# Kernel optimization log

Measured on AMD Instinct MI355X. Metric: run time of the kernel, lower is better.

The kernel has to match this reference:

```python
import jax, jax.numpy as jnp
import numpy as np

IN_FEATURES = 4096
LOCAL_FEATURES = 128
KERNEL_SIZE = 64
STRIDE = 32
FOLD_NUM = (IN_FEATURES - KERNEL_SIZE) // STRIDE + 1  # 127
BATCH = 4096


def setup_inputs() -> dict:
    key = jax.random.key(0)
    kx, kw, kb = jax.random.split(key, 3)
    x = jax.random.normal(kx, (BATCH, IN_FEATURES), dtype=jnp.float32)
    # Per-window linear weights: torch Linear weight is [out, in] = [local_features, kernel_size]
    bound = 1.0 / np.sqrt(KERNEL_SIZE)
    W = jax.random.uniform(kw, (FOLD_NUM, LOCAL_FEATURES, KERNEL_SIZE),
                           dtype=jnp.float32, minval=-bound, maxval=bound)
    b = jax.random.uniform(kb, (FOLD_NUM, LOCAL_FEATURES),
                           dtype=jnp.float32, minval=-bound, maxval=bound)
    return {"x": x, "W": W, "b": b}


def reference(x, W, b) -> jnp.ndarray:
    # Unfold: windows[f, k] = x[:, f*stride + k] -> [B, FOLD_NUM, KERNEL_SIZE]
    idx = jnp.arange(FOLD_NUM)[:, None] * STRIDE + jnp.arange(KERNEL_SIZE)[None, :]
    windows = x[:, idx]  # [B, F, K]
    # Batched per-window linear: out[b, f, l] = sum_k windows[b,f,k] * W[f,l,k] + b[f,l]
    out = jnp.einsum('bfk,flk->bfl', windows, W) + b[None, :, :]
    # torch.cat along dim 1 over fold index == reshape [B, F*L]
    return out.reshape(x.shape[0], FOLD_NUM * LOCAL_FEATURES)
```

## Files before the change

kernel.cpp:

```cpp
#include <hip/hip_runtime.h>
#include <hip/hip_bf16.h>

#define IN_F 4096
#define LOCAL_F 128
#define KSZ 64
#define STRIDE_ 32
#define FOLDS 127
#define BATCH_ 4096
#define OUT_F (FOLDS * LOCAL_F)
#define WN (FOLDS * LOCAL_F * KSZ)

#define BM 64
#define NF 4
#define XCOLS (NF * STRIDE_ + (KSZ - STRIDE_))
#define LDSP 168

typedef __attribute__((ext_vector_type(8))) short bf16x8;
typedef __attribute__((ext_vector_type(8))) unsigned short u16x8;
typedef __attribute__((ext_vector_type(4))) float f32x4;

__device__ __forceinline__ unsigned short f2bf(float f) {
    unsigned u = __builtin_bit_cast(unsigned, f);
    u += 0x7fffu + ((u >> 16) & 1u);
    return (unsigned short)(u >> 16);
}

__global__ __launch_bounds__(256)
void wprep_kernel(const float* __restrict__ W, unsigned short* __restrict__ Wbf) {
    int i = (blockIdx.x * 256 + threadIdx.x) * 8;
    if (i >= WN) return;
    float4 a = *reinterpret_cast<const float4*>(W + i);
    float4 c = *reinterpret_cast<const float4*>(W + i + 4);
    u16x8 s;
    s[0] = f2bf(a.x); s[1] = f2bf(a.y); s[2] = f2bf(a.z); s[3] = f2bf(a.w);
    s[4] = f2bf(c.x); s[5] = f2bf(c.y); s[6] = f2bf(c.z); s[7] = f2bf(c.w);
    *reinterpret_cast<u16x8*>(Wbf + i) = s;
}

template<bool WB>
__global__ __launch_bounds__(256, 2)
void local_linear_kernel(const float* __restrict__ x,
                         const float* __restrict__ Wf32,
                         const unsigned short* __restrict__ Wbf,
                         const float* __restrict__ b,
                         float* __restrict__ out) {
    __shared__ unsigned short xs[BM][LDSP];

    const int bg = blockIdx.x;
    const int fg = blockIdx.y;
    const int row0 = bg * BM;
    const int col0 = fg * (NF * STRIDE_);

    const int t = threadIdx.x;

    #pragma unroll
    for (int it = 0; it < (BM * (XCOLS / 4)) / 256; ++it) {
        int i  = t + it * 256;
        int r  = i / (XCOLS / 4);
        int c4 = i - r * (XCOLS / 4);
        int gcol = col0 + c4 * 4;
        float4 v = make_float4(0.f, 0.f, 0.f, 0.f);
        if (gcol < IN_F) {
            v = *reinterpret_cast<const float4*>(x + (size_t)(row0 + r) * IN_F + gcol);
        }
        ushort4 s;
        s.x = f2bf(v.x); s.y = f2bf(v.y); s.z = f2bf(v.z); s.w = f2bf(v.w);
        *reinterpret_cast<ushort4*>(&xs[r][c4 * 4]) = s;
    }
    __syncthreads();

    const int wave = t >> 6;
    const int lane = t & 63;
    const int f = fg * NF + wave;
    if (f >= FOLDS) return;

    const int l16 = lane & 15;
    const int g   = lane >> 4;

    f32x4 acc[4][8];
    #pragma unroll
    for (int mt = 0; mt < 4; ++mt)
        #pragma unroll
        for (int nt = 0; nt < 8; ++nt)
            acc[mt][nt] = (f32x4){0.f, 0.f, 0.f, 0.f};

    const int fcol = wave * STRIDE_;

    #pragma unroll
    for (int ks = 0; ks < 2; ++ks) {
        bf16x8 wf[8];
        #pragma unroll
        for (int nt = 0; nt < 8; ++nt) {
            if (WB) {
                wf[nt] = *reinterpret_cast<const bf16x8*>(
                    Wbf + ((size_t)f * LOCAL_F + nt * 16 + l16) * KSZ + ks * 32 + g * 8);
            } else {
                const float* p = Wf32 + ((size_t)f * LOCAL_F + nt * 16 + l16) * KSZ + ks * 32 + g * 8;
                float4 va = *reinterpret_cast<const float4*>(p);
                float4 vb = *reinterpret_cast<const float4*>(p + 4);
                bf16x8 w8;
                w8[0] = (short)f2bf(va.x); w8[1] = (short)f2bf(va.y);
                w8[2] = (short)f2bf(va.z); w8[3] = (short)f2bf(va.w);
                w8[4] = (short)f2bf(vb.x); w8[5] = (short)f2bf(vb.y);
                w8[6] = (short)f2bf(vb.z); w8[7] = (short)f2bf(vb.w);
                wf[nt] = w8;
            }
        }
        bf16x8 af[4];
        #pragma unroll
        for (int mt = 0; mt < 4; ++mt) {
            af[mt] = *reinterpret_cast<const bf16x8*>(&xs[mt * 16 + l16][fcol + ks * 32 + g * 8]);
        }
        #pragma unroll
        for (int mt = 0; mt < 4; ++mt)
            #pragma unroll
            for (int nt = 0; nt < 8; ++nt)
                acc[mt][nt] = __builtin_amdgcn_mfma_f32_16x16x32_bf16(wf[nt], af[mt], acc[mt][nt], 0, 0, 0);
    }

    f32x4 bv[8];
    #pragma unroll
    for (int nt = 0; nt < 8; ++nt)
        bv[nt] = *reinterpret_cast<const f32x4*>(b + (size_t)f * LOCAL_F + nt * 16 + 4 * g);

    #pragma unroll
    for (int mt = 0; mt < 4; ++mt) {
        float* orow = out + (size_t)(row0 + mt * 16 + l16) * OUT_F + f * LOCAL_F + 4 * g;
        #pragma unroll
        for (int nt = 0; nt < 8; ++nt) {
            f32x4 v = acc[mt][nt] + bv[nt];
            *reinterpret_cast<f32x4*>(orow + nt * 16) = v;
        }
    }
}

extern "C" void kernel_launch(void* const* d_in, const int* in_sizes, int n_in,
                              void* d_out, int out_size, void* d_ws, size_t ws_size,
                              hipStream_t stream) {
    const float* x = (const float*)d_in[0];
    const float* W = (const float*)d_in[1];
    const float* b = (const float*)d_in[2];
    float* out = (float*)d_out;
    dim3 grid(BATCH_ / BM, (FOLDS + NF - 1) / NF);

    if (ws_size >= (size_t)WN * sizeof(unsigned short)) {
        unsigned short* Wbf = (unsigned short*)d_ws;
        wprep_kernel<<<(WN / 8 + 255) / 256, 256, 0, stream>>>(W, Wbf);
        local_linear_kernel<true><<<grid, 256, 0, stream>>>(x, W, Wbf, b, out);
    } else {
        local_linear_kernel<false><<<grid, 256, 0, stream>>>(x, W, nullptr, b, out);
    }
}
```

Baseline: 117.7 us.

## Split each fold across two waves, halve folds per block, use nontemporal stores

Each block now covers 2 folds instead of 4, and each fold's 128 output features are split across two waves of 64 features each. This halves the accumulator registers per wave, and the launch bound is raised to 4 blocks per CU to get more occupancy and latency hiding. Output stores become nontemporal to avoid polluting the cache with the large streamed output. The trade-off is more redundant x loading and bf16 conversion, since the x overlap between neighbouring folds is now shared by fewer folds per block. The fp32-weight fallback path is removed and the workspace is assumed to be large enough.

New measurement: 103.0 us. -12.5%, faster.

```diff
diff --git a/kernel.cpp b/kernel.cpp
--- a/kernel.cpp
+++ b/kernel.cpp
@@ -11,9 +11,9 @@
 #define WN (FOLDS * LOCAL_F * KSZ)
 
 #define BM 64
-#define NF 4
+#define NF 2
 #define XCOLS (NF * STRIDE_ + (KSZ - STRIDE_))
-#define LDSP 168
+#define LDSP 104
 
 typedef __attribute__((ext_vector_type(8))) short bf16x8;
 typedef __attribute__((ext_vector_type(8))) unsigned short u16x8;
@@ -37,10 +37,8 @@
     *reinterpret_cast<u16x8*>(Wbf + i) = s;
 }
 
-template<bool WB>
-__global__ __launch_bounds__(256, 2)
+__global__ __launch_bounds__(256, 4)
 void local_linear_kernel(const float* __restrict__ x,
-                         const float* __restrict__ Wf32,
                          const unsigned short* __restrict__ Wbf,
                          const float* __restrict__ b,
                          float* __restrict__ out) {
@@ -71,65 +69,53 @@
 
     const int wave = t >> 6;
     const int lane = t & 63;
-    const int f = fg * NF + wave;
+    const int fold = wave >> 1;
+    const int h    = wave & 1;
+    const int f = fg * NF + fold;
     if (f >= FOLDS) return;
 
     const int l16 = lane & 15;
     const int g   = lane >> 4;
 
-    f32x4 acc[4][8];
+    f32x4 acc[4][4];
     #pragma unroll
     for (int mt = 0; mt < 4; ++mt)
         #pragma unroll
-        for (int nt = 0; nt < 8; ++nt)
+        for (int nt = 0; nt < 4; ++nt)
             acc[mt][nt] = (f32x4){0.f, 0.f, 0.f, 0.f};
 
-    const int fcol = wave * STRIDE_;
+    const int fcol = fold * STRIDE_;
+    const unsigned short* Wf = Wbf + (size_t)f * (LOCAL_F * KSZ) + (h * 4 * 16) * KSZ;
 
     #pragma unroll
     for (int ks = 0; ks < 2; ++ks) {
-        bf16x8 wf[8];
+        bf16x8 wf[4];
         #pragma unroll
-        for (int nt = 0; nt < 8; ++nt) {
-            if (WB) {
-                wf[nt] = *reinterpret_cast<const bf16x8*>(
-                    Wbf + ((size_t)f * LOCAL_F + nt * 16 + l16) * KSZ + ks * 32 + g * 8);
-            } else {
-                const float* p = Wf32 + ((size_t)f * LOCAL_F + nt * 16 + l16) * KSZ + ks * 32 + g * 8;
-                float4 va = *reinterpret_cast<const float4*>(p);
-                float4 vb = *reinterpret_cast<const float4*>(p + 4);
-                bf16x8 w8;
-                w8[0] = (short)f2bf(va.x); w8[1] = (short)f2bf(va.y);
-                w8[2] = (short)f2bf(va.z); w8[3] = (short)f2bf(va.w);
-                w8[4] = (short)f2bf(vb.x); w8[5] = (short)f2bf(vb.y);
-                w8[6] = (short)f2bf(vb.z); w8[7] = (short)f2bf(vb.w);
-                wf[nt] = w8;
-            }
-        }
+        for (int nt = 0; nt < 4; ++nt)
+            wf[nt] = *reinterpret_cast<const bf16x8*>(Wf + (nt * 16 + l16) * KSZ + ks * 32 + g * 8);
         bf16x8 af[4];
         #pragma unroll
-        for (int mt = 0; mt < 4; ++mt) {
+        for (int mt = 0; mt < 4; ++mt)
             af[mt] = *reinterpret_cast<const bf16x8*>(&xs[mt * 16 + l16][fcol + ks * 32 + g * 8]);
-        }
         #pragma unroll
         for (int mt = 0; mt < 4; ++mt)
             #pragma unroll
-            for (int nt = 0; nt < 8; ++nt)
+            for (int nt = 0; nt < 4; ++nt)
                 acc[mt][nt] = __builtin_amdgcn_mfma_f32_16x16x32_bf16(wf[nt], af[mt], acc[mt][nt], 0, 0, 0);
     }
 
-    f32x4 bv[8];
+    f32x4 bv[4];
     #pragma unroll
-    for (int nt = 0; nt < 8; ++nt)
-        bv[nt] = *reinterpret_cast<const f32x4*>(b + (size_t)f * LOCAL_F + nt * 16 + 4 * g);
+    for (int nt = 0; nt < 4; ++nt)
+        bv[nt] = *reinterpret_cast<const f32x4*>(b + (size_t)f * LOCAL_F + h * 64 + nt * 16 + 4 * g);
 
     #pragma unroll
     for (int mt = 0; mt < 4; ++mt) {
-        float* orow = out + (size_t)(row0 + mt * 16 + l16) * OUT_F + f * LOCAL_F + 4 * g;
+        float* orow = out + (size_t)(row0 + mt * 16 + l16) * OUT_F + f * LOCAL_F + h * 64 + 4 * g;
         #pragma unroll
-        for (int nt = 0; nt < 8; ++nt) {
+        for (int nt = 0; nt < 4; ++nt) {
             f32x4 v = acc[mt][nt] + bv[nt];
-            *reinterpret_cast<f32x4*>(orow + nt * 16) = v;
+            __builtin_nontemporal_store(v, reinterpret_cast<f32x4*>(orow + nt * 16));
         }
     }
 }
@@ -141,13 +127,9 @@
     const float* W = (const float*)d_in[1];
     const float* b = (const float*)d_in[2];
     float* out = (float*)d_out;
+    unsigned short* Wbf = (unsigned short*)d_ws;
+
+    wprep_kernel<<<(WN / 8 + 255) / 256, 256, 0, stream>>>(W, Wbf);
     dim3 grid(BATCH_ / BM, (FOLDS + NF - 1) / NF);
-
-    if (ws_size >= (size_t)WN * sizeof(unsigned short)) {
-        unsigned short* Wbf = (unsigned short*)d_ws;
-        wprep_kernel<<<(WN / 8 + 255) / 256, 256, 0, stream>>>(W, Wbf);
-        local_linear_kernel<true><<<grid, 256, 0, stream>>>(x, W, Wbf, b, out);
-    } else {
-        local_linear_kernel<false><<<grid, 256, 0, stream>>>(x, W, nullptr, b, out);
-    }
+    local_linear_kernel<<<grid, 256, 0, stream>>>(x, Wbf, b, out);
 }
```
